# Performance work log

Measured on AMD Instinct MI355X. Metric: run time of the kernel, lower is better.

Reference implementation:

```python
import jax, jax.numpy as jnp
import numpy as np

D_MODEL, D_KEY, N_HEADS = 256, 32, 8
B, T1, T2 = 4, 2048, 2048


def setup_inputs() -> dict:
    key = jax.random.key(0)
    ks = jax.random.split(key, 12)
    s = 1.0 / np.sqrt(D_MODEL)
    inp = {
        "key_input": jax.random.normal(ks[0], (B, T1, D_MODEL), jnp.float32),
        "query_input": jax.random.normal(ks[1], (B, T2, D_MODEL), jnp.float32),
        "value_input": jax.random.normal(ks[2], (B, T1, D_MODEL), jnp.float32),
        "attention_mask": jnp.ones((B, T1, T2), dtype=jnp.bool_),  # unused by the module, kept for API fidelity
        "WK_w": jax.random.uniform(ks[3], (D_KEY * N_HEADS, D_MODEL), jnp.float32, -s, s),
        "WK_b": jax.random.uniform(ks[4], (D_KEY * N_HEADS,), jnp.float32, -s, s),
        "WQ_w": jax.random.uniform(ks[5], (D_KEY * N_HEADS, D_MODEL), jnp.float32, -s, s),
        "WQ_b": jax.random.uniform(ks[6], (D_KEY * N_HEADS,), jnp.float32, -s, s),
        "WV_w": jax.random.uniform(ks[7], (D_MODEL * N_HEADS, D_MODEL), jnp.float32, -s, s),
        "WV_b": jax.random.uniform(ks[8], (D_MODEL * N_HEADS,), jnp.float32, -s, s),
        "WO_w": jax.random.uniform(ks[9], (D_MODEL, D_MODEL * N_HEADS), jnp.float32, -1.0 / np.sqrt(D_MODEL * N_HEADS), 1.0 / np.sqrt(D_MODEL * N_HEADS)),
        "WO_b": jax.random.uniform(ks[10], (D_MODEL,), jnp.float32, -1.0 / np.sqrt(D_MODEL * N_HEADS), 1.0 / np.sqrt(D_MODEL * N_HEADS)),
    }
    return inp


def reference(key_input, query_input, value_input, attention_mask,
              WK_w, WK_b, WQ_w, WQ_b, WV_w, WV_b, WO_w, WO_b):
    b, t1, dm = key_input.shape
    t2 = query_input.shape[1]
    h, dk = N_HEADS, D_KEY
    # projections
    k = key_input @ WK_w.T + WK_b      # [b, t1, h*dk]
    q = query_input @ WQ_w.T + WQ_b    # [b, t2, h*dk]
    v = value_input @ WV_w.T + WV_b    # [b, t1, h*dm] (per-head value dim == d_model)
    # head split: channel index c = head*dk + feat (head outer), matching torch reshapes
    k = k.reshape(b, t1, h, dk)
    q = q.reshape(b, t2, h, dk)
    v = v.reshape(b, t1, h, dm)
    # scores: NO 1/sqrt(dk) scaling and NO masking (faithful to source; mask arg unused)
    scores = jnp.einsum('bshk,bqhk->bhsq', k, q)      # [b, h, t1, t2]
    attn = jax.nn.softmax(scores, axis=2)             # softmax over KEY axis (torch dim=1 of [t1,t2])
    emb = jnp.einsum('bshd,bhsq->bqdh', v, attn)      # [b, t2, dm, h]
    emb = emb.reshape(b, t2, dm * h)                  # flatten (d_model outer, head inner)
    return emb @ WO_w.T + WO_b                        # [b, t2, d_model]
```

## Files before the change

### kernel.cpp

```cpp
#include <hip/hip_runtime.h>

typedef __attribute__((ext_vector_type(8))) short short8;
typedef __attribute__((ext_vector_type(4))) short short4v;
typedef __attribute__((ext_vector_type(4))) float float4v;
typedef __attribute__((ext_vector_type(4))) unsigned uint4v;
typedef __attribute__((ext_vector_type(2))) unsigned uint2v;

constexpr int T  = 2048;
constexpr int DM = 256;
constexpr int DK = 32;

__device__ inline short f2bf(float f) {
  unsigned u = __builtin_bit_cast(unsigned, f);
  u += 0x7fff + ((u >> 16) & 1);
  return (short)(u >> 16);
}

__device__ inline unsigned pk2(float a, float b) {
#if __has_builtin(__builtin_amdgcn_cvt_pk_bf16_f32)
  auto r = __builtin_amdgcn_cvt_pk_bf16_f32(a, b);
  return __builtin_bit_cast(unsigned, r);
#else
  unsigned ua = __builtin_bit_cast(unsigned, a);
  ua = (ua + 0x7fff + ((ua >> 16) & 1)) >> 16;
  unsigned ub = __builtin_bit_cast(unsigned, b);
  ub = (ub + 0x7fff + ((ub >> 16) & 1)) >> 16;
  return ua | (ub << 16);
#endif
}

__device__ inline short8 load8_bf(const float* __restrict__ p) {
  float4v a = *(const float4v*)p;
  float4v b = *(const float4v*)(p + 4);
  uint4v u;
  u[0] = pk2(a[0], a[1]); u[1] = pk2(a[2], a[3]);
  u[2] = pk2(b[0], b[1]); u[3] = pk2(b[2], b[3]);
  return __builtin_bit_cast(short8, u);
}
__device__ inline short8 load8_bf(const short* __restrict__ p) {
  return *(const short8*)p;
}
__device__ inline void storeC(short* C, long idx, float v) { C[idx] = f2bf(v); }
__device__ inline void storeC(float* C, long idx, float v) { C[idx] = v; }

template<typename TA, typename TB, typename TC, int MODE>
__global__ __launch_bounds__(256)
void gemm_nt(const TA* __restrict__ A, const TB* __restrict__ Bw,
             const float* __restrict__ bias, TC* __restrict__ C,
             int M, int N, int K) {
  __shared__ __align__(16) short As[128][40];
  __shared__ __align__(16) short Bs[128][40];

  const int tid  = threadIdx.x;
  const int wave = tid >> 6, lane = tid & 63;
  const int l15  = lane & 15, quad = lane >> 4;
  const int wm   = (wave & 1) * 64, wn = (wave >> 1) * 64;
  const long Abase = (long)blockIdx.x * 128;
  const long Bbase = (long)blockIdx.y * 128;

  float4v acc[4][4];
  for (int i = 0; i < 4; i++)
    for (int j = 0; j < 4; j++)
      for (int r = 0; r < 4; r++) acc[i][j][r] = 0.f;

  const int srow = tid >> 2;
  const int sc8  = (tid & 3) * 8;

  for (int k0 = 0; k0 < K; k0 += 32) {
    __syncthreads();
    for (int i = 0; i < 2; i++) {
      int row = srow + i * 64;
      *(short8*)&As[row][sc8] = load8_bf(A  + (Abase + row) * K + k0 + sc8);
      *(short8*)&Bs[row][sc8] = load8_bf(Bw + (Bbase + row) * K + k0 + sc8);
    }
    __syncthreads();
    short8 af[4], bfr[4];
    for (int ms = 0; ms < 4; ms++) af[ms]  = *(const short8*)&As[wm + ms*16 + l15][quad*8];
    for (int ns = 0; ns < 4; ns++) bfr[ns] = *(const short8*)&Bs[wn + ns*16 + l15][quad*8];
    for (int ms = 0; ms < 4; ms++)
      for (int ns = 0; ns < 4; ns++)
        acc[ms][ns] = __builtin_amdgcn_mfma_f32_16x16x32_bf16(af[ms], bfr[ns], acc[ms][ns], 0, 0, 0);
  }

  for (int ms = 0; ms < 4; ms++) {
    int rowl = wm + ms*16 + quad*4;
    for (int ns = 0; ns < 4; ns++) {
      int col = (int)Bbase + wn + ns*16 + l15;
      if (MODE == 0) {
        float bv = bias[col];
        for (int r = 0; r < 4; r++) {
          long row = Abase + rowl + r;
          storeC(C, row * (long)N + col, acc[ms][ns][r] + bv);
        }
      } else {
        int bidx = col >> 11, scol = col & 2047;
        for (int r = 0; r < 4; r++) {
          long m = Abase + rowl + r;
          storeC(C, ((long)bidx * 2048 + m) * 2048 + scol, acc[ms][ns][r] + bias[m]);
        }
      }
    }
  }
}

template<typename TA, typename TB, typename TC, bool DUAL>
__global__ __launch_bounds__(256)
void gemm_nt64(const TA* __restrict__ A, const TB* __restrict__ Bw,
               const float* __restrict__ bias, TC* __restrict__ C,
               const TA* __restrict__ A1, const TB* __restrict__ Bw1,
               const float* __restrict__ bias1, TC* __restrict__ C1,
               float scale1, int M, int N, int K) {
  __shared__ __align__(16) short As[128][40];
  __shared__ __align__(16) short Bs[64][40];

  float oscale = 1.0f;
  if (DUAL && blockIdx.z == 1) { A = A1; Bw = Bw1; bias = bias1; C = C1; oscale = scale1; }

  const int tid  = threadIdx.x;
  const int wave = tid >> 6, lane = tid & 63;
  const int l15  = lane & 15, quad = lane >> 4;
  const int wm   = (wave & 1) * 64, wn = (wave >> 1) * 32;
  const long Abase = (long)blockIdx.x * 128;
  const long Bbase = (long)blockIdx.y * 64;

  float4v acc[4][2];
  for (int i = 0; i < 4; i++)
    for (int j = 0; j < 2; j++)
      for (int r = 0; r < 4; r++) acc[i][j][r] = 0.f;

  const int srow = tid >> 2;
  const int sc8  = (tid & 3) * 8;

  for (int k0 = 0; k0 < K; k0 += 32) {
    __syncthreads();
    for (int i = 0; i < 2; i++) {
      int row = srow + i * 64;
      *(short8*)&As[row][sc8] = load8_bf(A + (Abase + row) * K + k0 + sc8);
    }
    *(short8*)&Bs[srow][sc8] = load8_bf(Bw + (Bbase + srow) * K + k0 + sc8);
    __syncthreads();
    short8 af[4], bfr[2];
    for (int ms = 0; ms < 4; ms++) af[ms]  = *(const short8*)&As[wm + ms*16 + l15][quad*8];
    for (int ns = 0; ns < 2; ns++) bfr[ns] = *(const short8*)&Bs[wn + ns*16 + l15][quad*8];
    for (int ms = 0; ms < 4; ms++)
      for (int ns = 0; ns < 2; ns++)
        acc[ms][ns] = __builtin_amdgcn_mfma_f32_16x16x32_bf16(af[ms], bfr[ns], acc[ms][ns], 0, 0, 0);
  }

  for (int ms = 0; ms < 4; ms++) {
    int rowl = wm + ms*16 + quad*4;
    for (int ns = 0; ns < 2; ns++) {
      int col = (int)Bbase + wn + ns*16 + l15;
      float bv = bias[col];
      for (int r = 0; r < 4; r++) {
        long row = Abase + rowl + r;
        storeC(C, row * (long)N + col, (acc[ms][ns][r] + bv) * oscale);
      }
    }
  }
}

__global__ __launch_bounds__(256)
void gemm_sk(const short* __restrict__ A, const float* __restrict__ Bw,
             float* __restrict__ C) {
  __shared__ __align__(16) short As[128][40];
  __shared__ __align__(16) short Bs[64][40];

  const int tid  = threadIdx.x;
  const int wave = tid >> 6, lane = tid & 63;
  const int l15  = lane & 15, quad = lane >> 4;
  const int wm   = (wave & 1) * 64, wn = (wave >> 1) * 32;
  const long Abase = (long)blockIdx.x * 128;
  const long Bbase = (long)blockIdx.y * 64;
  const int  kbase = blockIdx.z * 1024;
  const int  N = 256, K = 2048;

  float4v acc[4][2];
  for (int i = 0; i < 4; i++)
    for (int j = 0; j < 2; j++)
      for (int r = 0; r < 4; r++) acc[i][j][r] = 0.f;

  const int srow = tid >> 2;
  const int sc8  = (tid & 3) * 8;

  for (int k0 = kbase; k0 < kbase + 1024; k0 += 32) {
    __syncthreads();
    for (int i = 0; i < 2; i++) {
      int row = srow + i * 64;
      *(short8*)&As[row][sc8] = load8_bf(A + (Abase + row) * K + k0 + sc8);
    }
    *(short8*)&Bs[srow][sc8] = load8_bf(Bw + (Bbase + srow) * K + k0 + sc8);
    __syncthreads();
    short8 af[4], bfr[2];
    for (int ms = 0; ms < 4; ms++) af[ms]  = *(const short8*)&As[wm + ms*16 + l15][quad*8];
    for (int ns = 0; ns < 2; ns++) bfr[ns] = *(const short8*)&Bs[wn + ns*16 + l15][quad*8];
    for (int ms = 0; ms < 4; ms++)
      for (int ns = 0; ns < 2; ns++)
        acc[ms][ns] = __builtin_amdgcn_mfma_f32_16x16x32_bf16(af[ms], bfr[ns], acc[ms][ns], 0, 0, 0);
  }

  for (int ms = 0; ms < 4; ms++) {
    int rowl = wm + ms*16 + quad*4;
    for (int ns = 0; ns < 2; ns++) {
      int col = (int)Bbase + wn + ns*16 + l15;
      for (int r = 0; r < 4; r++) {
        long row = Abase + rowl + r;
        atomicAdd(&C[row * (long)N + col], acc[ms][ns][r]);
      }
    }
  }
}

__global__ void bias_fill(const float* __restrict__ b, float* __restrict__ out) {
  int idx = blockIdx.x * 256 + threadIdx.x;
  out[idx] = b[idx & 255];
}

__global__ void permute_wo(const float* __restrict__ src, float* __restrict__ dst) {
  int idx = blockIdx.x * 256 + threadIdx.x;
  int n = idx >> 11, c = idx & 2047;
  int h = c >> 8, d = c & 255;
  dst[idx] = src[n * 2048 + d * 8 + h];
}

__global__ __launch_bounds__(256, 2)
void attn_kernel(const short* __restrict__ Kp, const short* __restrict__ Qp,
                 const short* __restrict__ Vt, short* __restrict__ emb) {
  __shared__ __align__(16) short Pt[128][136];
  __shared__ __align__(16) float psum[128][4];

  const int tid  = threadIdx.x;
  const int wave = tid >> 6, lane = tid & 63;
  const int l15  = lane & 15, quad = lane >> 4;

  const int L  = blockIdx.x;
  const int h  = L & 7;
  const int b  = (L >> 3) & 3;
  const int q0 = (L >> 5) * 128;

  const short* Kbh = Kp + (long)b * T * DM + h * DK;
  const short* Qbh = Qp + (long)b * T * DM + h * DK;
  const short* Vbh = Vt + ((long)b * 2048 + h * 256) * 2048;

  float4v acc[4][8];
  for (int i = 0; i < 4; i++)
    for (int j = 0; j < 8; j++)
      for (int r = 0; r < 4; r++) acc[i][j][r] = 0.f;

  float ps[8];
  for (int i = 0; i < 8; i++) ps[i] = 0.f;

  short8 qf[8];
  for (int qs = 0; qs < 8; qs++)
    qf[qs] = *(const short8*)(Qbh + (long)(q0 + qs*16 + l15) * DM + quad*8);

  for (int it = 0; it < T / 128; it++) {
    const int s0 = it * 128;

    for (int ss = 0; ss < 2; ss++) {
      short8 kf = *(const short8*)(Kbh + (long)(s0 + wave*32 + ss*16 + l15) * DM + quad*8);
      for (int qs = 0; qs < 8; qs++) {
        float4v z = {0.f, 0.f, 0.f, 0.f};
        float4v st = __builtin_amdgcn_mfma_f32_16x16x32_bf16(kf, qf[qs], z, 0, 0, 0);
        float p0 = exp2f(st[0]), p1 = exp2f(st[1]);
        float p2 = exp2f(st[2]), p3 = exp2f(st[3]);
        ps[qs] += (p0 + p1) + (p2 + p3);
        uint2v pb; pb[0] = pk2(p0, p1); pb[1] = pk2(p2, p3);
        *(uint2v*)&Pt[qs*16 + l15][wave*32 + ss*16 + quad*4] = pb;
      }
    }
    __syncthreads();

    for (int ks = 0; ks < 4; ks++) {
      short8 pf[8];
      for (int ns = 0; ns < 8; ns++)
        pf[ns] = *(const short8*)&Pt[ns*16 + l15][ks*32 + quad*8];
      for (int ms = 0; ms < 4; ms++) {
        short8 vf = *(const short8*)(Vbh + (long)(wave*64 + ms*16 + l15) * 2048
                                     + s0 + ks*32 + quad*8);
        for (int ns = 0; ns < 8; ns++)
          acc[ms][ns] = __builtin_amdgcn_mfma_f32_16x16x32_bf16(vf, pf[ns], acc[ms][ns], 0, 0, 0);
      }
    }
    __syncthreads();
  }

  for (int qs = 0; qs < 8; qs++) {
    ps[qs] += __shfl_xor(ps[qs], 16, 64);
    ps[qs] += __shfl_xor(ps[qs], 32, 64);
  }
  if (lane < 16)
    for (int qs = 0; qs < 8; qs++) psum[qs*16 + lane][wave] = ps[qs];
  __syncthreads();

  for (int ns = 0; ns < 8; ns++) {
    float4v sv = *(const float4v*)&psum[ns*16 + l15][0];
    float rl = 1.0f / (sv[0] + sv[1] + sv[2] + sv[3]);
    long rowbase = ((long)(b * T + q0 + ns*16 + l15)) * 2048 + h * 256;
    for (int ms = 0; ms < 4; ms++) {
      uint2v ob;
      ob[0] = pk2(acc[ms][ns][0] * rl, acc[ms][ns][1] * rl);
      ob[1] = pk2(acc[ms][ns][2] * rl, acc[ms][ns][3] * rl);
      *(uint2v*)(emb + rowbase + wave*64 + ms*16 + quad*4) = ob;
    }
  }
}

extern "C" void kernel_launch(void* const* d_in, const int* in_sizes, int n_in,
                              void* d_out, int out_size, void* d_ws, size_t ws_size,
                              hipStream_t stream) {
  const float* key_x   = (const float*)d_in[0];
  const float* query_x = (const float*)d_in[1];
  const float* value_x = (const float*)d_in[2];
  const float* WK_w = (const float*)d_in[4];
  const float* WK_b = (const float*)d_in[5];
  const float* WQ_w = (const float*)d_in[6];
  const float* WQ_b = (const float*)d_in[7];
  const float* WV_w = (const float*)d_in[8];
  const float* WV_b = (const float*)d_in[9];
  const float* WO_w = (const float*)d_in[10];
  const float* WO_b = (const float*)d_in[11];

  char* ws = (char*)d_ws;
  short* Kp   = (short*)(ws);
  short* Qp   = (short*)(ws + (4u  << 20));
  short* Vt   = (short*)(ws + (8u  << 20));
  short* embp = (short*)(ws + (40u << 20));
  float* WOp  = (float*)(ws + (72u << 20));
  float* outp = (float*)d_out;

  const float L2E = 1.44269504f;

  permute_wo<<<2048, 256, 0, stream>>>(WO_w, WOp);
  gemm_nt64<float, float, short, true><<<dim3(64, 4, 2), 256, 0, stream>>>(
      key_x, WK_w, WK_b, Kp, query_x, WQ_w, WQ_b, Qp, L2E, 8192, 256, 256);
  gemm_nt<float, float, short, 1><<<dim3(16, 64), 256, 0, stream>>>(
      WV_w, value_x, WV_b, Vt, 2048, 8192, 256);
  attn_kernel<<<dim3(512), 256, 0, stream>>>(Kp, Qp, Vt, embp);
  bias_fill<<<8192, 256, 0, stream>>>(WO_b, outp);
  gemm_sk<<<dim3(64, 4, 2), 256, 0, stream>>>(embp, WOp, outp);
}
```

Baseline: 346.9 us.

## Double-buffer attention P tile and replace atomic split-K with partial-sum reduction

```diff
diff --git a/kernel.cpp b/kernel.cpp
--- a/kernel.cpp
+++ b/kernel.cpp
@@ -161,8 +161,8 @@
 }
 
 __global__ __launch_bounds__(256)
-void gemm_sk(const short* __restrict__ A, const float* __restrict__ Bw,
-             float* __restrict__ C) {
+void gemm_fin(const short* __restrict__ A, const short* __restrict__ Bw,
+              float* __restrict__ partial) {
   __shared__ __align__(16) short As[128][40];
   __shared__ __align__(16) short Bs[64][40];
 
@@ -172,8 +172,9 @@
   const int wm   = (wave & 1) * 64, wn = (wave >> 1) * 32;
   const long Abase = (long)blockIdx.x * 128;
   const long Bbase = (long)blockIdx.y * 64;
-  const int  kbase = blockIdx.z * 1024;
+  const int  kbase = blockIdx.z * 512;
   const int  N = 256, K = 2048;
+  float* Cz = partial + (long)blockIdx.z * 8192 * 256;
 
   float4v acc[4][2];
   for (int i = 0; i < 4; i++)
@@ -183,13 +184,13 @@
   const int srow = tid >> 2;
   const int sc8  = (tid & 3) * 8;
 
-  for (int k0 = kbase; k0 < kbase + 1024; k0 += 32) {
+  for (int k0 = kbase; k0 < kbase + 512; k0 += 32) {
     __syncthreads();
     for (int i = 0; i < 2; i++) {
       int row = srow + i * 64;
-      *(short8*)&As[row][sc8] = load8_bf(A + (Abase + row) * K + k0 + sc8);
-    }
-    *(short8*)&Bs[srow][sc8] = load8_bf(Bw + (Bbase + srow) * K + k0 + sc8);
+      *(short8*)&As[row][sc8] = *(const short8*)(A + (Abase + row) * K + k0 + sc8);
+    }
+    *(short8*)&Bs[srow][sc8] = *(const short8*)(Bw + (Bbase + srow) * K + k0 + sc8);
     __syncthreads();
     short8 af[4], bfr[2];
     for (int ms = 0; ms < 4; ms++) af[ms]  = *(const short8*)&As[wm + ms*16 + l15][quad*8];
@@ -205,28 +206,38 @@
       int col = (int)Bbase + wn + ns*16 + l15;
       for (int r = 0; r < 4; r++) {
         long row = Abase + rowl + r;
-        atomicAdd(&C[row * (long)N + col], acc[ms][ns][r]);
-      }
-    }
-  }
-}
-
-__global__ void bias_fill(const float* __restrict__ b, float* __restrict__ out) {
-  int idx = blockIdx.x * 256 + threadIdx.x;
-  out[idx] = b[idx & 255];
-}
-
-__global__ void permute_wo(const float* __restrict__ src, float* __restrict__ dst) {
+        Cz[row * (long)N + col] = acc[ms][ns][r];
+      }
+    }
+  }
+}
+
+__global__ void reduce_fin(const float* __restrict__ partial,
+                           const float* __restrict__ bias,
+                           float* __restrict__ out) {
+  const long P = 8192L * 256;
+  long i4 = ((long)blockIdx.x * 256 + threadIdx.x) * 4;
+  float4v s = *(const float4v*)(partial + i4);
+  float4v s1 = *(const float4v*)(partial + P + i4);
+  float4v s2 = *(const float4v*)(partial + 2*P + i4);
+  float4v s3 = *(const float4v*)(partial + 3*P + i4);
+  float4v bv = *(const float4v*)(bias + (i4 & 255));
+  float4v o;
+  for (int r = 0; r < 4; r++) o[r] = bv[r] + ((s[r] + s1[r]) + (s2[r] + s3[r]));
+  *(float4v*)(out + i4) = o;
+}
+
+__global__ void permute_wo(const float* __restrict__ src, short* __restrict__ dst) {
   int idx = blockIdx.x * 256 + threadIdx.x;
   int n = idx >> 11, c = idx & 2047;
   int h = c >> 8, d = c & 255;
-  dst[idx] = src[n * 2048 + d * 8 + h];
+  dst[idx] = f2bf(src[n * 2048 + d * 8 + h]);
 }
 
 __global__ __launch_bounds__(256, 2)
 void attn_kernel(const short* __restrict__ Kp, const short* __restrict__ Qp,
                  const short* __restrict__ Vt, short* __restrict__ emb) {
-  __shared__ __align__(16) short Pt[128][136];
+  __shared__ __align__(16) short Pt[2][128][136];
   __shared__ __align__(16) float psum[128][4];
 
   const int tid  = threadIdx.x;
@@ -254,27 +265,36 @@
   for (int qs = 0; qs < 8; qs++)
     qf[qs] = *(const short8*)(Qbh + (long)(q0 + qs*16 + l15) * DM + quad*8);
 
-  for (int it = 0; it < T / 128; it++) {
-    const int s0 = it * 128;
-
+  auto computeSt = [&](int s0, int buf) {
     for (int ss = 0; ss < 2; ss++) {
       short8 kf = *(const short8*)(Kbh + (long)(s0 + wave*32 + ss*16 + l15) * DM + quad*8);
       for (int qs = 0; qs < 8; qs++) {
         float4v z = {0.f, 0.f, 0.f, 0.f};
         float4v st = __builtin_amdgcn_mfma_f32_16x16x32_bf16(kf, qf[qs], z, 0, 0, 0);
-        float p0 = exp2f(st[0]), p1 = exp2f(st[1]);
-        float p2 = exp2f(st[2]), p3 = exp2f(st[3]);
-        ps[qs] += (p0 + p1) + (p2 + p3);
-        uint2v pb; pb[0] = pk2(p0, p1); pb[1] = pk2(p2, p3);
-        *(uint2v*)&Pt[qs*16 + l15][wave*32 + ss*16 + quad*4] = pb;
-      }
-    }
-    __syncthreads();
-
+        short4v pb;
+        float s4 = 0.f;
+        for (int r = 0; r < 4; r++) {
+          float p = exp2f(st[r]);
+          s4 += p;
+          pb[r] = f2bf(p);
+        }
+        ps[qs] += s4;
+        *(short4v*)&Pt[buf][qs*16 + l15][wave*32 + ss*16 + quad*4] = pb;
+      }
+    }
+  };
+
+  computeSt(0, 0);
+
+  for (int it = 0; it < T / 128; it++) {
+    const int buf = it & 1;
+    const int s0  = it * 128;
+    __syncthreads();
+    if (it < T / 128 - 1) computeSt(s0 + 128, buf ^ 1);
     for (int ks = 0; ks < 4; ks++) {
       short8 pf[8];
       for (int ns = 0; ns < 8; ns++)
-        pf[ns] = *(const short8*)&Pt[ns*16 + l15][ks*32 + quad*8];
+        pf[ns] = *(const short8*)&Pt[buf][ns*16 + l15][ks*32 + quad*8];
       for (int ms = 0; ms < 4; ms++) {
         short8 vf = *(const short8*)(Vbh + (long)(wave*64 + ms*16 + l15) * 2048
                                      + s0 + ks*32 + quad*8);
@@ -282,7 +302,6 @@
           acc[ms][ns] = __builtin_amdgcn_mfma_f32_16x16x32_bf16(vf, pf[ns], acc[ms][ns], 0, 0, 0);
       }
     }
-    __syncthreads();
   }
 
   for (int qs = 0; qs < 8; qs++) {
@@ -298,10 +317,9 @@
     float rl = 1.0f / (sv[0] + sv[1] + sv[2] + sv[3]);
     long rowbase = ((long)(b * T + q0 + ns*16 + l15)) * 2048 + h * 256;
     for (int ms = 0; ms < 4; ms++) {
-      uint2v ob;
-      ob[0] = pk2(acc[ms][ns][0] * rl, acc[ms][ns][1] * rl);
-      ob[1] = pk2(acc[ms][ns][2] * rl, acc[ms][ns][3] * rl);
-      *(uint2v*)(emb + rowbase + wave*64 + ms*16 + quad*4) = ob;
+      short4v ob;
+      for (int r = 0; r < 4; r++) ob[r] = f2bf(acc[ms][ns][r] * rl);
+      *(short4v*)(emb + rowbase + wave*64 + ms*16 + quad*4) = ob;
     }
   }
 }
@@ -326,17 +344,18 @@
   short* Qp   = (short*)(ws + (4u  << 20));
   short* Vt   = (short*)(ws + (8u  << 20));
   short* embp = (short*)(ws + (40u << 20));
-  float* WOp  = (float*)(ws + (72u << 20));
+  short* WOpb = (short*)(ws + (72u << 20));
+  float* part = (float*)(ws);
   float* outp = (float*)d_out;
 
   const float L2E = 1.44269504f;
 
-  permute_wo<<<2048, 256, 0, stream>>>(WO_w, WOp);
+  permute_wo<<<2048, 256, 0, stream>>>(WO_w, WOpb);
   gemm_nt64<float, float, short, true><<<dim3(64, 4, 2), 256, 0, stream>>>(
       key_x, WK_w, WK_b, Kp, query_x, WQ_w, WQ_b, Qp, L2E, 8192, 256, 256);
   gemm_nt<float, float, short, 1><<<dim3(16, 64), 256, 0, stream>>>(
       WV_w, value_x, WV_b, Vt, 2048, 8192, 256);
   attn_kernel<<<dim3(512), 256, 0, stream>>>(Kp, Qp, Vt, embp);
-  bias_fill<<<8192, 256, 0, stream>>>(WO_b, outp);
-  gemm_sk<<<dim3(64, 4, 2), 256, 0, stream>>>(embp, WOp, outp);
-}
+  gemm_fin<<<dim3(64, 4, 4), 256, 0, stream>>>(embp, WOpb, part);
+  reduce_fin<<<2048, 256, 0, stream>>>(part, WO_b, outp);
+}
```

Result: faster. 310.6 us (-10.5%).

## Merge projection, permute and bias launches into one kernel and double-buffer attention P tile

Applied to the files above, without the earlier changes.

```diff
diff --git a/kernel.cpp b/kernel.cpp
--- a/kernel.cpp
+++ b/kernel.cpp
@@ -29,6 +29,14 @@
 #endif
 }
 
+__device__ inline float fexp2(float x) {
+#if __has_builtin(__builtin_amdgcn_exp2f)
+  return __builtin_amdgcn_exp2f(x);
+#else
+  return exp2f(x);
+#endif
+}
+
 __device__ inline short8 load8_bf(const float* __restrict__ p) {
   float4v a = *(const float4v*)p;
   float4v b = *(const float4v*)(p + 4);
@@ -37,91 +45,20 @@
   u[2] = pk2(b[0], b[1]); u[3] = pk2(b[2], b[3]);
   return __builtin_bit_cast(short8, u);
 }
-__device__ inline short8 load8_bf(const short* __restrict__ p) {
-  return *(const short8*)p;
-}
-__device__ inline void storeC(short* C, long idx, float v) { C[idx] = f2bf(v); }
-__device__ inline void storeC(float* C, long idx, float v) { C[idx] = v; }
-
-template<typename TA, typename TB, typename TC, int MODE>
-__global__ __launch_bounds__(256)
-void gemm_nt(const TA* __restrict__ A, const TB* __restrict__ Bw,
-             const float* __restrict__ bias, TC* __restrict__ C,
-             int M, int N, int K) {
-  __shared__ __align__(16) short As[128][40];
-  __shared__ __align__(16) short Bs[128][40];
-
-  const int tid  = threadIdx.x;
-  const int wave = tid >> 6, lane = tid & 63;
-  const int l15  = lane & 15, quad = lane >> 4;
-  const int wm   = (wave & 1) * 64, wn = (wave >> 1) * 64;
-  const long Abase = (long)blockIdx.x * 128;
-  const long Bbase = (long)blockIdx.y * 128;
-
-  float4v acc[4][4];
-  for (int i = 0; i < 4; i++)
-    for (int j = 0; j < 4; j++)
-      for (int r = 0; r < 4; r++) acc[i][j][r] = 0.f;
-
-  const int srow = tid >> 2;
-  const int sc8  = (tid & 3) * 8;
-
-  for (int k0 = 0; k0 < K; k0 += 32) {
-    __syncthreads();
-    for (int i = 0; i < 2; i++) {
-      int row = srow + i * 64;
-      *(short8*)&As[row][sc8] = load8_bf(A  + (Abase + row) * K + k0 + sc8);
-      *(short8*)&Bs[row][sc8] = load8_bf(Bw + (Bbase + row) * K + k0 + sc8);
-    }
-    __syncthreads();
-    short8 af[4], bfr[4];
-    for (int ms = 0; ms < 4; ms++) af[ms]  = *(const short8*)&As[wm + ms*16 + l15][quad*8];
-    for (int ns = 0; ns < 4; ns++) bfr[ns] = *(const short8*)&Bs[wn + ns*16 + l15][quad*8];
-    for (int ms = 0; ms < 4; ms++)
-      for (int ns = 0; ns < 4; ns++)
-        acc[ms][ns] = __builtin_amdgcn_mfma_f32_16x16x32_bf16(af[ms], bfr[ns], acc[ms][ns], 0, 0, 0);
-  }
-
-  for (int ms = 0; ms < 4; ms++) {
-    int rowl = wm + ms*16 + quad*4;
-    for (int ns = 0; ns < 4; ns++) {
-      int col = (int)Bbase + wn + ns*16 + l15;
-      if (MODE == 0) {
-        float bv = bias[col];
-        for (int r = 0; r < 4; r++) {
-          long row = Abase + rowl + r;
-          storeC(C, row * (long)N + col, acc[ms][ns][r] + bv);
-        }
-      } else {
-        int bidx = col >> 11, scol = col & 2047;
-        for (int r = 0; r < 4; r++) {
-          long m = Abase + rowl + r;
-          storeC(C, ((long)bidx * 2048 + m) * 2048 + scol, acc[ms][ns][r] + bias[m]);
-        }
-      }
-    }
-  }
-}
-
-template<typename TA, typename TB, typename TC, bool DUAL>
-__global__ __launch_bounds__(256)
-void gemm_nt64(const TA* __restrict__ A, const TB* __restrict__ Bw,
-               const float* __restrict__ bias, TC* __restrict__ C,
-               const TA* __restrict__ A1, const TB* __restrict__ Bw1,
-               const float* __restrict__ bias1, TC* __restrict__ C1,
-               float scale1, int M, int N, int K) {
-  __shared__ __align__(16) short As[128][40];
-  __shared__ __align__(16) short Bs[64][40];
-
-  float oscale = 1.0f;
-  if (DUAL && blockIdx.z == 1) { A = A1; Bw = Bw1; bias = bias1; C = C1; oscale = scale1; }
-
+
+__device__ inline void gemm_body64(const float* __restrict__ A,
+                                   const float* __restrict__ Bw,
+                                   const float* __restrict__ bias,
+                                   short* __restrict__ C,
+                                   float oscale, int bx, int by,
+                                   int K, int N, int mode,
+                                   short (&As)[128][40], short (&Bs)[64][40]) {
   const int tid  = threadIdx.x;
   const int wave = tid >> 6, lane = tid & 63;
   const int l15  = lane & 15, quad = lane >> 4;
   const int wm   = (wave & 1) * 64, wn = (wave >> 1) * 32;
-  const long Abase = (long)blockIdx.x * 128;
-  const long Bbase = (long)blockIdx.y * 64;
+  const long Abase = (long)bx * 128;
+  const long Bbase = (long)by * 64;
 
   float4v acc[4][2];
   for (int i = 0; i < 4; i++)
@@ -151,17 +88,69 @@
     int rowl = wm + ms*16 + quad*4;
     for (int ns = 0; ns < 2; ns++) {
       int col = (int)Bbase + wn + ns*16 + l15;
-      float bv = bias[col];
-      for (int r = 0; r < 4; r++) {
-        long row = Abase + rowl + r;
-        storeC(C, row * (long)N + col, (acc[ms][ns][r] + bv) * oscale);
+      if (mode == 0) {
+        float bv = bias[col];
+        for (int r = 0; r < 4; r++) {
+          long row = Abase + rowl + r;
+          C[row * (long)N + col] = f2bf((acc[ms][ns][r] + bv) * oscale);
+        }
+      } else {
+        int bidx = col >> 11, scol = col & 2047;
+        for (int r = 0; r < 4; r++) {
+          long m = Abase + rowl + r;
+          C[((long)bidx * 2048 + m) * 2048 + scol] = f2bf(acc[ms][ns][r] + bias[m]);
+        }
       }
     }
   }
 }
 
 __global__ __launch_bounds__(256)
-void gemm_sk(const short* __restrict__ A, const float* __restrict__ Bw,
+void mega_proj(const float* __restrict__ key_x, const float* __restrict__ query_x,
+               const float* __restrict__ value_x,
+               const float* __restrict__ WK_w, const float* __restrict__ WK_b,
+               const float* __restrict__ WQ_w, const float* __restrict__ WQ_b,
+               const float* __restrict__ WV_w, const float* __restrict__ WV_b,
+               const float* __restrict__ WO_w, const float* __restrict__ WO_b,
+               short* __restrict__ Kp, short* __restrict__ Qp,
+               short* __restrict__ Vt, short* __restrict__ WOpb,
+               float* __restrict__ outp) {
+  __shared__ __align__(16) short As[128][40];
+  __shared__ __align__(16) short Bs[64][40];
+
+  const int gb = blockIdx.x;
+  if (gb < 512) {
+    const int z  = gb >> 8;
+    const int bx = gb & 63, by = (gb >> 6) & 3;
+    const float L2E = 1.44269504f;
+    if (z == 0)
+      gemm_body64(key_x,   WK_w, WK_b, Kp, 1.0f, bx, by, 256, 256, 0, As, Bs);
+    else
+      gemm_body64(query_x, WQ_w, WQ_b, Qp, L2E,  bx, by, 256, 256, 0, As, Bs);
+  } else if (gb < 2560) {
+    const int sub = gb - 512;
+    const int bx = sub & 15, by = sub >> 4;
+    gemm_body64(WV_w, value_x, WV_b, Vt, 1.0f, bx, by, 256, 8192, 1, As, Bs);
+  } else if (gb < 2624) {
+    const int p = gb - 2560;
+    for (int i = 0; i < 32; i++) {
+      int idx = p * 8192 + i * 256 + threadIdx.x;
+      int n = idx >> 11, c = idx & 2047;
+      int h = c >> 8, d = c & 255;
+      WOpb[idx] = f2bf(WO_w[n * 2048 + d * 8 + h]);
+    }
+  } else {
+    const int p = gb - 2624;
+    for (long i4 = ((long)p * 256 + threadIdx.x) * 4; i4 < 8192L * 256;
+         i4 += 32L * 256 * 4) {
+      float4v bv = *(const float4v*)(WO_b + (i4 & 255));
+      *(float4v*)(outp + i4) = bv;
+    }
+  }
+}
+
+__global__ __launch_bounds__(256)
+void gemm_sk(const short* __restrict__ A, const short* __restrict__ Bw,
              float* __restrict__ C) {
   __shared__ __align__(16) short As[128][40];
   __shared__ __align__(16) short Bs[64][40];
@@ -187,9 +176,9 @@
     __syncthreads();
     for (int i = 0; i < 2; i++) {
       int row = srow + i * 64;
-      *(short8*)&As[row][sc8] = load8_bf(A + (Abase + row) * K + k0 + sc8);
-    }
-    *(short8*)&Bs[srow][sc8] = load8_bf(Bw + (Bbase + srow) * K + k0 + sc8);
+      *(short8*)&As[row][sc8] = *(const short8*)(A + (Abase + row) * K + k0 + sc8);
+    }
+    *(short8*)&Bs[srow][sc8] = *(const short8*)(Bw + (Bbase + srow) * K + k0 + sc8);
     __syncthreads();
     short8 af[4], bfr[2];
     for (int ms = 0; ms < 4; ms++) af[ms]  = *(const short8*)&As[wm + ms*16 + l15][quad*8];
@@ -211,22 +200,10 @@
   }
 }
 
-__global__ void bias_fill(const float* __restrict__ b, float* __restrict__ out) {
-  int idx = blockIdx.x * 256 + threadIdx.x;
-  out[idx] = b[idx & 255];
-}
-
-__global__ void permute_wo(const float* __restrict__ src, float* __restrict__ dst) {
-  int idx = blockIdx.x * 256 + threadIdx.x;
-  int n = idx >> 11, c = idx & 2047;
-  int h = c >> 8, d = c & 255;
-  dst[idx] = src[n * 2048 + d * 8 + h];
-}
-
 __global__ __launch_bounds__(256, 2)
 void attn_kernel(const short* __restrict__ Kp, const short* __restrict__ Qp,
                  const short* __restrict__ Vt, short* __restrict__ emb) {
-  __shared__ __align__(16) short Pt[128][136];
+  __shared__ __align__(16) short Pt[2][128][136];
   __shared__ __align__(16) float psum[128][4];
 
   const int tid  = threadIdx.x;
@@ -254,27 +231,32 @@
   for (int qs = 0; qs < 8; qs++)
     qf[qs] = *(const short8*)(Qbh + (long)(q0 + qs*16 + l15) * DM + quad*8);
 
-  for (int it = 0; it < T / 128; it++) {
-    const int s0 = it * 128;
-
+  auto computeSt = [&](int s0, int buf) {
     for (int ss = 0; ss < 2; ss++) {
       short8 kf = *(const short8*)(Kbh + (long)(s0 + wave*32 + ss*16 + l15) * DM + quad*8);
       for (int qs = 0; qs < 8; qs++) {
         float4v z = {0.f, 0.f, 0.f, 0.f};
         float4v st = __builtin_amdgcn_mfma_f32_16x16x32_bf16(kf, qf[qs], z, 0, 0, 0);
-        float p0 = exp2f(st[0]), p1 = exp2f(st[1]);
-        float p2 = exp2f(st[2]), p3 = exp2f(st[3]);
+        float p0 = fexp2(st[0]), p1 = fexp2(st[1]);
+        float p2 = fexp2(st[2]), p3 = fexp2(st[3]);
         ps[qs] += (p0 + p1) + (p2 + p3);
         uint2v pb; pb[0] = pk2(p0, p1); pb[1] = pk2(p2, p3);
-        *(uint2v*)&Pt[qs*16 + l15][wave*32 + ss*16 + quad*4] = pb;
+        *(uint2v*)&Pt[buf][qs*16 + l15][wave*32 + ss*16 + quad*4] = pb;
       }
     }
-    __syncthreads();
-
+  };
+
+  computeSt(0, 0);
+
+  for (int it = 0; it < T / 128; it++) {
+    const int buf = it & 1;
+    const int s0  = it * 128;
+    __syncthreads();
+    if (it < T / 128 - 1) computeSt(s0 + 128, buf ^ 1);
     for (int ks = 0; ks < 4; ks++) {
       short8 pf[8];
       for (int ns = 0; ns < 8; ns++)
-        pf[ns] = *(const short8*)&Pt[ns*16 + l15][ks*32 + quad*8];
+        pf[ns] = *(const short8*)&Pt[buf][ns*16 + l15][ks*32 + quad*8];
       for (int ms = 0; ms < 4; ms++) {
         short8 vf = *(const short8*)(Vbh + (long)(wave*64 + ms*16 + l15) * 2048
                                      + s0 + ks*32 + quad*8);
@@ -282,7 +264,6 @@
           acc[ms][ns] = __builtin_amdgcn_mfma_f32_16x16x32_bf16(vf, pf[ns], acc[ms][ns], 0, 0, 0);
       }
     }
-    __syncthreads();
   }
 
   for (int qs = 0; qs < 8; qs++) {
@@ -326,17 +307,12 @@
   short* Qp   = (short*)(ws + (4u  << 20));
   short* Vt   = (short*)(ws + (8u  << 20));
   short* embp = (short*)(ws + (40u << 20));
-  float* WOp  = (float*)(ws + (72u << 20));
+  short* WOpb = (short*)(ws + (72u << 20));
   float* outp = (float*)d_out;
 
-  const float L2E = 1.44269504f;
-
-  permute_wo<<<2048, 256, 0, stream>>>(WO_w, WOp);
-  gemm_nt64<float, float, short, true><<<dim3(64, 4, 2), 256, 0, stream>>>(
-      key_x, WK_w, WK_b, Kp, query_x, WQ_w, WQ_b, Qp, L2E, 8192, 256, 256);
-  gemm_nt<float, float, short, 1><<<dim3(16, 64), 256, 0, stream>>>(
-      WV_w, value_x, WV_b, Vt, 2048, 8192, 256);
+  mega_proj<<<2656, 256, 0, stream>>>(key_x, query_x, value_x,
+                                      WK_w, WK_b, WQ_w, WQ_b, WV_w, WV_b,
+                                      WO_w, WO_b, Kp, Qp, Vt, WOpb, outp);
   attn_kernel<<<dim3(512), 256, 0, stream>>>(Kp, Qp, Vt, embp);
-  bias_fill<<<8192, 256, 0, stream>>>(WO_b, outp);
-  gemm_sk<<<dim3(64, 4, 2), 256, 0, stream>>>(embp, WOp, outp);
-}
+  gemm_sk<<<dim3(64, 4, 2), 256, 0, stream>>>(embp, WOpb, outp);
+}
```

Result: faster. 314.8 us (-9.3%).
